# Optimization experiments

Measured on AMD Instinct MI355X. Metric: run time of the kernel, lower is better.

The kernel has to match this reference:

```python
import jax, jax.numpy as jnp
import numpy as np

B, CIN, G, H, HW, WMIX = 128, 64, 8, 14, 16, 16  # batch, in-ch, groups, spatial, mixed width


def setup_inputs() -> dict:
    key = jax.random.key(0)
    k1, k2, k3 = jax.random.split(key, 3)
    x = jax.random.normal(k1, (B, CIN, G, H, H), dtype=jnp.float32)
    w_conv = jax.random.normal(k2, (G, 3, 3, 32), dtype=jnp.float32)   # weights[0]
    w_mix = jax.random.normal(k3, (CIN, WMIX), dtype=jnp.float32)       # weights[1]
    return {"x": x, "w_conv": w_conv, "w_mix": w_mix}


def _unfold3(t, axis, size):
    # torch F.unfold with kernel (3,1), padding (1,0) along `axis`: zero-pad by 1
    # and stack the 3 shifted windows as a new axis inserted at `axis`.
    pad = [(0, 0)] * t.ndim
    pad[axis] = (1, 1)
    p = jnp.pad(t, pad)
    slices = []
    for k in range(3):
        idx = [slice(None)] * t.ndim
        idx[axis] = slice(k, k + size)
        slices.append(p[tuple(idx)])
    return jnp.stack(slices, axis=axis)


def reference(x, w_conv, w_mix):
    # channel mix: (B, 64, 8, 14, 14) x (64, 16) -> (B, 8, 14, 14, 16)
    t4 = jnp.einsum('kjmnl,ji->kmnli', x, w_mix)
    # first unfold along H (axis 3): (B, 8, 14, 3, 14, 16)
    u1 = _unfold3(t4, 3, H)
    # second unfold along H (now axis 4): (B, 8, 14, 3, 3, 14, 16)
    u2 = _unfold3(u1, 4, H)
    # permute (0,1,2,5,4,3,6) -> (B, 8, 14, 14, 3, 3, 16)
    t5 = jnp.transpose(u2, (0, 1, 2, 5, 4, 3, 6))
    # conv channel mix: contract group(8) and both 3-taps -> (B, 14, 14, 16, 32)
    t6 = jnp.einsum('mlonikp,likj->monpj', t5, w_conv)
    # (B, 14, 14, 32, 16) -> (B, 14, 14, 512)
    t7 = jnp.transpose(t6, (0, 1, 2, 4, 3)).reshape(B, H, H, 512)
    t7 = jnp.roll(t7, 1, axis=1)  # shift_direction fixed to +1
    return jnp.transpose(t7, (0, 3, 1, 2))  # (B, 512, 14, 14)
```

## Files before the change

### kernel.cpp

```cpp
#include <hip/hip_runtime.h>

static constexpr int NB   = 128;
static constexpr int NCIN = 64;
static constexpr int NG   = 8;
static constexpr int NH   = 14;
static constexpr int NP   = 16;
static constexpr int HH   = NH * NH;
static constexpr int LROW = 20;

static constexpr int OFF_W2 = 0;
static constexpr int OFF_WC = 1280;
static constexpr int OFF_T4 = 1792;
static constexpr int OFF_XS = 4352;
static constexpr int LDS_FLOATS = 8384;

__global__ __launch_bounds__(256) void fused_kernel(const float* __restrict__ x,
                                                    const float* __restrict__ wconv,
                                                    const float* __restrict__ wmix,
                                                    float* __restrict__ out) {
    __shared__ __align__(16) float lds[LDS_FLOATS];
    float*  w2s = lds + OFF_W2;
    float*  wcs = lds + OFF_WC;
    float*  t4s = lds + OFF_T4;
    float4* xs4 = reinterpret_cast<float4*>(lds + OFF_XS);

    const int tid   = threadIdx.x;
    const int b     = blockIdx.x / NH;
    const int o     = blockIdx.x % NH;
    const int o_src = (o + NH - 1) % NH;

    const float* xb = x + (size_t)b * (NCIN * NG * HH) + o_src * NH;

    float xr[14];
#pragma unroll
    for (int r = 0; r < 14; r++) {
        int idx = r * 256 + tid;
        int j   = idx / 112;
        int gl  = idx % 112;
        xr[r] = xb[(size_t)j * (NG * HH) + (gl / 14) * HH + (gl % 14)];
    }

#pragma unroll
    for (int r = 0; r < 5; r++) {
        int idx = r * 256 + tid;
        int g   = idx / 160;
        int di  = (idx / 32) % 5;
        int j   = idx % 32;
        int ilo = di > 2 ? di - 2 : 0;
        int ihi = di < 2 ? di : 2;
        float s = 0.f;
        for (int i = ilo; i <= ihi; i++) {
            int k = di - i;
            s += wconv[((g * 3 + i) * 3 + k) * 32 + j];
        }
        w2s[idx] = s;
    }
#pragma unroll
    for (int r = 0; r < 2; r++) {
        int idx = r * 256 + tid;
        int sel = idx / 256;
        int g   = (idx / 32) % 8;
        int j   = idx % 32;
        wcs[idx] = wconv[(g * 9 + (sel ? 6 : 2)) * 32 + j];
    }
#pragma unroll
    for (int r = 0; r < 3; r++) {
        int idx = r * 256 + tid;
        int gp  = idx / 6;
        int s   = idx % 6;
        int l2  = (s < 2) ? s : (14 + s);
        t4s[gp * LROW + l2] = 0.f;
    }
#pragma unroll
    for (int r = 0; r < 14; r++) {
        int idx  = r * 256 + tid;
        int j    = idx / 112;
        int gl   = idx % 112;
        int glst = gl + (gl >> 3);
        lds[OFF_XS + (((j >> 2) * 126 + glst) << 2) + (j & 3)] = xr[r];
    }
    __syncthreads();

#pragma unroll
    for (int r = 0; r < 14; r++) {
        int idx = r * 256 + tid;
        int j   = 32 + idx / 112;
        int gl  = idx % 112;
        xr[r] = xb[(size_t)j * (NG * HH) + (gl / 14) * HH + (gl % 14)];
    }

    const int  wv   = tid >> 6;
    const int  glB  = ((wv & 1) << 6) + (tid & 63);
    const bool bact = (glB < 112);
    const int  p0   = __builtin_amdgcn_readfirstlane((tid >> 7) << 3);
    const int  glst = glB + (glB >> 3);

    float am[8] = {0.f, 0.f, 0.f, 0.f, 0.f, 0.f, 0.f, 0.f};

    if (bact) {
#pragma unroll
        for (int j4 = 0; j4 < 8; j4++) {
            float4 xq = xs4[j4 * 126 + glst];
#pragma unroll
            for (int pp = 0; pp < 8; pp++) {
                const int p = p0 + pp;
                am[pp] += xq.x * wmix[(j4 * 4 + 0) * NP + p]
                        + xq.y * wmix[(j4 * 4 + 1) * NP + p]
                        + xq.z * wmix[(j4 * 4 + 2) * NP + p]
                        + xq.w * wmix[(j4 * 4 + 3) * NP + p];
            }
        }
    }
    __syncthreads();
#pragma unroll
    for (int r = 0; r < 14; r++) {
        int idx  = r * 256 + tid;
        int j    = idx / 112;
        int gl   = idx % 112;
        int glst2 = gl + (gl >> 3);
        lds[OFF_XS + (((j >> 2) * 126 + glst2) << 2) + (j & 3)] = xr[r];
    }
    __syncthreads();

    if (bact) {
        const float* wm1 = wmix + 32 * NP;
#pragma unroll
        for (int j4 = 0; j4 < 8; j4++) {
            float4 xq = xs4[j4 * 126 + glst];
#pragma unroll
            for (int pp = 0; pp < 8; pp++) {
                const int p = p0 + pp;
                am[pp] += xq.x * wm1[(j4 * 4 + 0) * NP + p]
                        + xq.y * wm1[(j4 * 4 + 1) * NP + p]
                        + xq.z * wm1[(j4 * 4 + 2) * NP + p]
                        + xq.w * wm1[(j4 * 4 + 3) * NP + p];
            }
        }
        int g = glB / 14, l = glB % 14;
#pragma unroll
        for (int pp = 0; pp < 8; pp++) {
            t4s[(g * 16 + p0 + pp) * LROW + l + 2] = am[pp];
        }
    }
    __syncthreads();

    const int p  = tid & 15;
    const int jh = tid >> 4;
    const int jb = jh * 2;

    float acc[NH][2];
#pragma unroll
    for (int n = 0; n < NH; n++) { acc[n][0] = 0.f; acc[n][1] = 0.f; }

    for (int g = 0; g < NG; g++) {
        float row[LROW];
        const float* rp = &t4s[(g * 16 + p) * LROW];
#pragma unroll
        for (int q = 0; q < 5; q++) {
            float4 v = *reinterpret_cast<const float4*>(rp + q * 4);
            row[q * 4 + 0] = v.x; row[q * 4 + 1] = v.y;
            row[q * 4 + 2] = v.z; row[q * 4 + 3] = v.w;
        }
#pragma unroll
        for (int di = 0; di < 5; di++) {
            float2 w = *reinterpret_cast<const float2*>(&w2s[(g * 5 + di) * 32 + jb]);
#pragma unroll
            for (int n = 0; n < NH; n++) {
                float rv = row[n + di];
                acc[n][0] += rv * w.x;
                acc[n][1] += rv * w.y;
            }
        }
        float2 c0 = *reinterpret_cast<const float2*>(&wcs[g * 32 + jb]);
        float2 c1 = *reinterpret_cast<const float2*>(&wcs[256 + g * 32 + jb]);
        float r2 = row[2], r15 = row[15];
        acc[0][0]  -= r2  * c0.x; acc[0][1]  -= r2  * c0.y;
        acc[13][0] -= r15 * c1.x; acc[13][1] -= r15 * c1.y;
    }

    __syncthreads();

#pragma unroll
    for (int jj = 0; jj < 2; jj++) {
        int cl  = (jb + jj) * 16 + p;
        int rot = (cl >> 5) * 2;
        int sb  = cl * 15;
#pragma unroll
        for (int n = 0; n < NH; n++) {
            int rn = n + rot;
            rn -= (rn >= 15) ? 15 : 0;
            rn -= (rn >= 15) ? 15 : 0;
            lds[sb + rn] = acc[n][jj];
        }
    }
    __syncthreads();

    float* ob = out + (size_t)b * 512 * HH + (size_t)o * NH;
#pragma unroll
    for (int r = 0; r < 28; r++) {
        int idx = r * 256 + tid;
        int c   = idx / 14;
        int n   = idx % 14;
        int rn  = n + (c >> 5) * 2;
        rn -= (rn >= 15) ? 15 : 0;
        rn -= (rn >= 15) ? 15 : 0;
        ob[(size_t)c * HH + n] = lds[c * 15 + rn];
    }
}

extern "C" void kernel_launch(void* const* d_in, const int* in_sizes, int n_in,
                              void* d_out, int out_size, void* d_ws, size_t ws_size,
                              hipStream_t stream) {
    const float* x     = (const float*)d_in[0];
    const float* wconv = (const float*)d_in[1];
    const float* wmix  = (const float*)d_in[2];
    float* out = (float*)d_out;
    (void)d_ws; (void)ws_size;

    fused_kernel<<<NB * NH, 256, 0, stream>>>(x, wconv, wmix, out);
}
```

Before: 140.8 us.

## Shrink LDS, coalesce x loads per lane, and vectorize output stores

The LDS layout is reordered so the x staging buffer aliases the weight region, which cuts LDS use, and the launch bound now asks for five blocks per SM. x loads become simple strided loads per lane, with 16 rows per thread and no div/mod per element. The conv weight pre-sums are computed from registers after the channel mix rather than before it. The output write now stores float2 pairs using a simplified rotation mapping. Together these aim to raise occupancy and trim index arithmetic and store instructions, at the cost of more register pressure from the occupancy hint.

```diff
diff --git a/kernel.cpp b/kernel.cpp
--- a/kernel.cpp
+++ b/kernel.cpp
@@ -8,20 +8,20 @@
 static constexpr int HH   = NH * NH;
 static constexpr int LROW = 20;
 
-static constexpr int OFF_W2 = 0;
-static constexpr int OFF_WC = 1280;
-static constexpr int OFF_T4 = 1792;
-static constexpr int OFF_XS = 4352;
-static constexpr int LDS_FLOATS = 8384;
-
-__global__ __launch_bounds__(256) void fused_kernel(const float* __restrict__ x,
-                                                    const float* __restrict__ wconv,
-                                                    const float* __restrict__ wmix,
-                                                    float* __restrict__ out) {
+static constexpr int OFF_T4 = 0;
+static constexpr int OFF_W2 = 2560;
+static constexpr int OFF_WC = 3840;
+static constexpr int OFF_XS = 2560;
+static constexpr int LDS_FLOATS = 7680;
+
+__global__ __launch_bounds__(256, 5) void fused_kernel(const float* __restrict__ x,
+                                                       const float* __restrict__ wconv,
+                                                       const float* __restrict__ wmix,
+                                                       float* __restrict__ out) {
     __shared__ __align__(16) float lds[LDS_FLOATS];
+    float*  t4s = lds + OFF_T4;
     float*  w2s = lds + OFF_W2;
     float*  wcs = lds + OFF_WC;
-    float*  t4s = lds + OFF_T4;
     float4* xs4 = reinterpret_cast<float4*>(lds + OFF_XS);
 
     const int tid   = threadIdx.x;
@@ -31,38 +31,28 @@
 
     const float* xb = x + (size_t)b * (NCIN * NG * HH) + o_src * NH;
 
-    float xr[14];
-#pragma unroll
-    for (int r = 0; r < 14; r++) {
-        int idx = r * 256 + tid;
-        int j   = idx / 112;
-        int gl  = idx % 112;
-        xr[r] = xb[(size_t)j * (NG * HH) + (gl / 14) * HH + (gl % 14)];
-    }
-
-#pragma unroll
-    for (int r = 0; r < 5; r++) {
-        int idx = r * 256 + tid;
-        int g   = idx / 160;
-        int di  = (idx / 32) % 5;
-        int j   = idx % 32;
-        int ilo = di > 2 ? di - 2 : 0;
-        int ihi = di < 2 ? di : 2;
-        float s = 0.f;
-        for (int i = ilo; i <= ihi; i++) {
-            int k = di - i;
-            s += wconv[((g * 3 + i) * 3 + k) * 32 + j];
-        }
-        w2s[idx] = s;
-    }
-#pragma unroll
-    for (int r = 0; r < 2; r++) {
-        int idx = r * 256 + tid;
-        int sel = idx / 256;
-        int g   = (idx / 32) % 8;
-        int j   = idx % 32;
-        wcs[idx] = wconv[(g * 9 + (sel ? 6 : 2)) * 32 + j];
-    }
+    const int  lane128 = tid & 127;
+    const bool xact    = lane128 < 112;
+    const int  jrow    = tid >> 7;
+    const int  gS      = lane128 / 14;
+    const int  lS      = lane128 % 14;
+    const int  glst    = lane128 + (lane128 >> 3);
+
+    float xr[16];
+    const float* xb0 = xb + (size_t)(jrow * 16) * (NG * HH) + gS * HH + lS;
+    if (xact) {
+#pragma unroll
+        for (int r = 0; r < 16; r++) xr[r] = xb0[(size_t)r * (NG * HH)];
+    }
+
+    const int gW = tid >> 5, jW = tid & 31;
+    float wv9[9];
+    {
+        const float* wp = wconv + (size_t)(gW * 9) * 32 + jW;
+#pragma unroll
+        for (int t = 0; t < 9; t++) wv9[t] = wp[t * 32];
+    }
+
 #pragma unroll
     for (int r = 0; r < 3; r++) {
         int idx = r * 256 + tid;
@@ -71,33 +61,25 @@
         int l2  = (s < 2) ? s : (14 + s);
         t4s[gp * LROW + l2] = 0.f;
     }
-#pragma unroll
-    for (int r = 0; r < 14; r++) {
-        int idx  = r * 256 + tid;
-        int j    = idx / 112;
-        int gl   = idx % 112;
-        int glst = gl + (gl >> 3);
-        lds[OFF_XS + (((j >> 2) * 126 + glst) << 2) + (j & 3)] = xr[r];
-    }
-    __syncthreads();
-
-#pragma unroll
-    for (int r = 0; r < 14; r++) {
-        int idx = r * 256 + tid;
-        int j   = 32 + idx / 112;
-        int gl  = idx % 112;
-        xr[r] = xb[(size_t)j * (NG * HH) + (gl / 14) * HH + (gl % 14)];
-    }
-
-    const int  wv   = tid >> 6;
-    const int  glB  = ((wv & 1) << 6) + (tid & 63);
-    const bool bact = (glB < 112);
-    const int  p0   = __builtin_amdgcn_readfirstlane((tid >> 7) << 3);
-    const int  glst = glB + (glB >> 3);
-
+
+    if (xact) {
+        float* xw = lds + OFF_XS + (jrow * 4 * 126 + glst) * 4;
+#pragma unroll
+        for (int r = 0; r < 16; r++)
+            xw[(r >> 2) * (126 * 4) + (r & 3)] = xr[r];
+    }
+    __syncthreads();
+
+    if (xact) {
+        const float* xb1 = xb0 + (size_t)32 * (NG * HH);
+#pragma unroll
+        for (int r = 0; r < 16; r++) xr[r] = xb1[(size_t)r * (NG * HH)];
+    }
+
+    const int p0 = __builtin_amdgcn_readfirstlane((tid >> 7) << 3);
     float am[8] = {0.f, 0.f, 0.f, 0.f, 0.f, 0.f, 0.f, 0.f};
 
-    if (bact) {
+    if (xact) {
 #pragma unroll
         for (int j4 = 0; j4 < 8; j4++) {
             float4 xq = xs4[j4 * 126 + glst];
@@ -112,17 +94,15 @@
         }
     }
     __syncthreads();
-#pragma unroll
-    for (int r = 0; r < 14; r++) {
-        int idx  = r * 256 + tid;
-        int j    = idx / 112;
-        int gl   = idx % 112;
-        int glst2 = gl + (gl >> 3);
-        lds[OFF_XS + (((j >> 2) * 126 + glst2) << 2) + (j & 3)] = xr[r];
-    }
-    __syncthreads();
-
-    if (bact) {
+    if (xact) {
+        float* xw = lds + OFF_XS + (jrow * 4 * 126 + glst) * 4;
+#pragma unroll
+        for (int r = 0; r < 16; r++)
+            xw[(r >> 2) * (126 * 4) + (r & 3)] = xr[r];
+    }
+    __syncthreads();
+
+    if (xact) {
         const float* wm1 = wmix + 32 * NP;
 #pragma unroll
         for (int j4 = 0; j4 < 8; j4++) {
@@ -136,11 +116,27 @@
                         + xq.w * wm1[(j4 * 4 + 3) * NP + p];
             }
         }
-        int g = glB / 14, l = glB % 14;
 #pragma unroll
         for (int pp = 0; pp < 8; pp++) {
-            t4s[(g * 16 + p0 + pp) * LROW + l + 2] = am[pp];
-        }
+            t4s[(gS * 16 + p0 + pp) * LROW + lS + 2] = am[pp];
+        }
+    }
+    __syncthreads();
+
+    {
+        float d0 = wv9[0];
+        float d1 = wv9[1] + wv9[3];
+        float d2 = wv9[2] + wv9[4] + wv9[6];
+        float d3 = wv9[5] + wv9[7];
+        float d4 = wv9[8];
+        float* wp2 = w2s + gW * 160 + jW;
+        wp2[0]   = d0;
+        wp2[32]  = d1;
+        wp2[64]  = d2;
+        wp2[96]  = d3;
+        wp2[128] = d4;
+        wcs[gW * 32 + jW]       = wv9[2];
+        wcs[256 + gW * 32 + jW] = wv9[6];
     }
     __syncthreads();
 
@@ -180,31 +176,41 @@
 
     __syncthreads();
 
-#pragma unroll
-    for (int jj = 0; jj < 2; jj++) {
-        int cl  = (jb + jj) * 16 + p;
-        int rot = (cl >> 5) * 2;
-        int sb  = cl * 15;
-#pragma unroll
-        for (int n = 0; n < NH; n++) {
-            int rn = n + rot;
-            rn -= (rn >= 15) ? 15 : 0;
-            rn -= (rn >= 15) ? 15 : 0;
-            lds[sb + rn] = acc[n][jj];
-        }
-    }
-    __syncthreads();
-
-    float* ob = out + (size_t)b * 512 * HH + (size_t)o * NH;
-#pragma unroll
-    for (int r = 0; r < 28; r++) {
-        int idx = r * 256 + tid;
-        int c   = idx / 14;
-        int n   = idx % 14;
-        int rn  = n + (c >> 5) * 2;
-        rn -= (rn >= 15) ? 15 : 0;
-        rn -= (rn >= 15) ? 15 : 0;
-        ob[(size_t)c * HH + n] = lds[c * 15 + rn];
+    {
+        int rotw = jh * 2;
+        rotw -= (rotw >= 14) ? 14 : 0;
+        rotw -= (rotw >= 14) ? 14 : 0;
+#pragma unroll
+        for (int jj = 0; jj < 2; jj++) {
+            int sb = ((jb + jj) * 16 + p) * 15;
+#pragma unroll
+            for (int n = 0; n < NH; n++) {
+                int rn = n + rotw;
+                rn -= (rn >= 14) ? 14 : 0;
+                lds[sb + rn] = acc[n][jj];
+            }
+        }
+    }
+    __syncthreads();
+
+    {
+        const int  k7   = tid & 7;
+        const bool kact = k7 < 7;
+        const int  cb   = tid >> 3;
+        float* ob = out + (size_t)b * 512 * HH + (size_t)o * NH;
+        if (kact) {
+#pragma unroll
+            for (int r = 0; r < 16; r++) {
+                int c   = cb + 32 * r;
+                int rot = (2 * r) % 14;
+                int rn  = 2 * k7 + rot;
+                rn -= (rn >= 14) ? 14 : 0;
+                float v0 = lds[c * 15 + rn];
+                float v1 = lds[c * 15 + rn + 1];
+                *reinterpret_cast<float2*>(ob + (size_t)c * HH + 2 * k7) =
+                    make_float2(v0, v1);
+            }
+        }
     }
 }
 
```

Result: faster. 131.7 us (-6.4%).
